# Performance work log

Hardware: AMD Instinct MI355X
Metric: run time of the kernel (lower is better)

Reference implementation:

```python
import jax, jax.numpy as jnp
from jax import lax
import numpy as np

BS, L, D, K, R, VOCAB = 4096, 200, 64, 4, 3, 100000
DROP = jnp.float32(-(1 << 31))


def squash(caps):
    # caps: (bs, K, D)
    n = jnp.linalg.norm(caps, axis=2, keepdims=True)   # (bs, K, 1)
    n2 = n * n
    return n2 / ((1.0 + n2) * n + 1e-9) * caps


def setup_inputs() -> dict:
    key = jax.random.key(0)
    ks = jax.random.split(key, 8)
    his = jax.random.randint(ks[0], (BS, L), 0, VOCAB)                     # item ids, 0 = pad
    E = jax.random.normal(ks[1], (VOCAB, D), dtype=jnp.float32)            # itemEmbeds.weight
    S = jax.random.normal(ks[2], (D, D), dtype=jnp.float32)                # bilinear map S
    B0 = jax.random.normal(ks[3], (K, L), dtype=jnp.float32)               # routing logits
    lim1 = 1.0 / np.sqrt(D)
    W1 = jax.random.uniform(ks[4], (D, 4 * D), jnp.float32, -lim1, lim1)   # dense1 (in, out)
    b1 = jax.random.uniform(ks[5], (4 * D,), jnp.float32, -lim1, lim1)
    lim2 = 1.0 / np.sqrt(4 * D)
    W2 = jax.random.uniform(ks[6], (4 * D, D), jnp.float32, -lim2, lim2)   # dense2 (in, out)
    b2 = jax.random.uniform(ks[7], (D,), jnp.float32, -lim2, lim2)
    return {"his": his, "E": E, "S": S, "B0": B0, "W1": W1, "b1": b1, "W2": W2, "b2": b2}


def reference(his, E, S, B0, W1, b1, W2, b2):
    bs = his.shape[0]
    # padding_idx=0 -> embedding row 0 is zero
    E = E.at[0].set(0.0)
    mask = (his != 0)[:, None, :]                       # (bs, 1, L), broadcasts over K
    hisP = jnp.einsum('bld,de->ble', E[his], S)         # (bs, L, D)
    hisPd = lax.stop_gradient(hisP)                     # routing updates run under no_grad
    B = jnp.broadcast_to(lax.stop_gradient(B0)[None], (bs, K, L))
    for _ in range(R - 1):
        W = jax.nn.softmax(jnp.where(mask, B, DROP), axis=2)   # (bs, K, L)
        caps = squash(jnp.einsum('bkl,bld->bkd', W, hisPd))
        B = B + jnp.einsum('bkd,bld->bkl', caps, hisPd)
    W = jax.nn.softmax(jnp.where(mask, B, DROP), axis=2)
    caps = squash(jnp.einsum('bkl,bld->bkd', W, hisP))         # differentiable last iter
    h = jax.nn.relu(jnp.einsum('bkd,df->bkf', caps, W1) + b1)
    return jnp.einsum('bkf,fd->bkd', h, W2) + b2               # (bs, K, D)
```

## Files before the change

kernel.cpp:

```cpp
#include <hip/hip_runtime.h>

#define LSEQ 200
#define KCAP 4
#define NVOC 100000

__global__ __launch_bounds__(256) void precompute_P(
    const float* __restrict__ E, const float* __restrict__ S,
    float* __restrict__ P)
{
    __shared__ __align__(16) float Sl[64 * 64];
    __shared__ __align__(16) float Et[64 * 16];
    const int tid = threadIdx.x;
    #pragma unroll
    for (int t = tid; t < 4096; t += 256) Sl[t] = S[t];
    const int vbase = blockIdx.x * 16;
    #pragma unroll
    for (int t = tid; t < 1024; t += 256) {
        int r = t >> 6, e = t & 63;
        Et[e * 16 + r] = E[(vbase + r) * 64 + e];
    }
    __syncthreads();
    const int d = tid & 63, q = tid >> 6;
    float a0 = 0.f, a1 = 0.f, a2 = 0.f, a3 = 0.f;
    #pragma unroll
    for (int e = 0; e < 64; e++) {
        float4 ev = *(const float4*)(Et + e * 16 + q * 4);
        float  s  = Sl[e * 64 + d];
        a0 = fmaf(ev.x, s, a0);
        a1 = fmaf(ev.y, s, a1);
        a2 = fmaf(ev.z, s, a2);
        a3 = fmaf(ev.w, s, a3);
    }
    const int v0 = vbase + q * 4;
    if (v0 == 0) a0 = 0.f;
    P[(v0 + 0) * 64 + d] = a0;
    P[(v0 + 1) * 64 + d] = a1;
    P[(v0 + 2) * 64 + d] = a2;
    P[(v0 + 3) * 64 + d] = a3;
}

__global__ __launch_bounds__(256, 2) void mind_row(
    const int*   __restrict__ his, const float* __restrict__ P,
    const float* __restrict__ B0,  const float* __restrict__ W1,
    const float* __restrict__ b1,  const float* __restrict__ W2,
    const float* __restrict__ b2,  float* __restrict__ out)
{
    __shared__ __align__(16) float hisPl[LSEQ * 65];
    __shared__ __align__(16) float W4[LSEQ * 4];
    __shared__ __align__(16) float Bm[KCAP * LSEQ];
    __shared__ __align__(16) float caps4[64 * 4];
    __shared__ __align__(16) float part[4 * 4 * 64];
    __shared__ float bigneg[LSEQ];
    __shared__ int   idxs[LSEQ];

    const int b    = blockIdx.x;
    const int tid  = threadIdx.x;
    const int lane = tid & 63;
    const int wv   = tid >> 6;

    for (int l = tid; l < LSEQ; l += 256) {
        int id = his[b * LSEQ + l];
        idxs[l]   = id;
        bigneg[l] = (id != 0) ? 0.f : -1e30f;
    }
    for (int t = tid; t < KCAP * LSEQ; t += 256) Bm[t] = B0[t];
    __syncthreads();

    float hp[50];
    #pragma unroll
    for (int i = 0; i < 50; i++) {
        int l = wv * 50 + i;
        float v = P[idxs[l] * 64 + lane];
        hp[i] = v;
        hisPl[l * 65 + lane] = v;
    }
    __syncthreads();

    for (int r = 0; r < 3; r++) {
        {
            const float* Bk = Bm + wv * LSEQ;
            float x0 = Bk[lane]       + bigneg[lane];
            float x1 = Bk[lane + 64]  + bigneg[lane + 64];
            float x2 = Bk[lane + 128] + bigneg[lane + 128];
            float x3 = (lane < 8) ? (Bk[lane + 192] + bigneg[lane + 192]) : -3.0e38f;
            float m = fmaxf(fmaxf(x0, x1), fmaxf(x2, x3));
            #pragma unroll
            for (int off = 32; off; off >>= 1) m = fmaxf(m, __shfl_xor(m, off, 64));
            float e0 = __expf(x0 - m), e1 = __expf(x1 - m), e2 = __expf(x2 - m);
            float e3 = (lane < 8) ? __expf(x3 - m) : 0.f;
            float s = e0 + e1 + e2 + e3;
            #pragma unroll
            for (int off = 32; off; off >>= 1) s += __shfl_xor(s, off, 64);
            float inv = 1.f / s;
            W4[lane * 4 + wv]         = e0 * inv;
            W4[(lane + 64) * 4 + wv]  = e1 * inv;
            W4[(lane + 128) * 4 + wv] = e2 * inv;
            if (lane < 8) W4[(lane + 192) * 4 + wv] = e3 * inv;
        }
        __syncthreads();

        {
            float a0 = 0, a1 = 0, a2 = 0, a3 = 0;
            #pragma unroll
            for (int i = 0; i < 50; i++) {
                int l = wv * 50 + i;
                float4 w = *(const float4*)(W4 + l * 4);
                float  v = hp[i];
                a0 = fmaf(w.x, v, a0);
                a1 = fmaf(w.y, v, a1);
                a2 = fmaf(w.z, v, a2);
                a3 = fmaf(w.w, v, a3);
            }
            part[wv * 256 + lane]       = a0;
            part[wv * 256 + 64 + lane]  = a1;
            part[wv * 256 + 128 + lane] = a2;
            part[wv * 256 + 192 + lane] = a3;
        }
        __syncthreads();

        {
            float c = part[wv * 64 + lane]       + part[256 + wv * 64 + lane]
                    + part[512 + wv * 64 + lane] + part[768 + wv * 64 + lane];
            float n2 = c * c;
            #pragma unroll
            for (int off = 32; off; off >>= 1) n2 += __shfl_xor(n2, off, 64);
            float n  = sqrtf(n2);
            float sc = n2 / ((1.f + n2) * n + 1e-9f);
            c *= sc;
            caps4[lane * 4 + wv] = c;
        }
        __syncthreads();

        if (r < 2) {
            if (tid < LSEQ) {
                const int l = tid;
                float d0 = 0, d1 = 0, d2 = 0, d3 = 0;
                #pragma unroll 8
                for (int d = 0; d < 64; d++) {
                    float  v = hisPl[l * 65 + d];
                    float4 c = *(const float4*)(caps4 + d * 4);
                    d0 = fmaf(c.x, v, d0);
                    d1 = fmaf(c.y, v, d1);
                    d2 = fmaf(c.z, v, d2);
                    d3 = fmaf(c.w, v, d3);
                }
                Bm[l]       += d0;
                Bm[200 + l] += d1;
                Bm[400 + l] += d2;
                Bm[600 + l] += d3;
            }
            __syncthreads();
        }
    }

    float* h4 = hisPl;
    {
        const int f = tid;
        float h0 = 0, h1 = 0, h2 = 0, h3 = 0;
        #pragma unroll 8
        for (int d = 0; d < 64; d++) {
            float  w = W1[d * 256 + f];
            float4 c = *(const float4*)(caps4 + d * 4);
            h0 = fmaf(c.x, w, h0);
            h1 = fmaf(c.y, w, h1);
            h2 = fmaf(c.z, w, h2);
            h3 = fmaf(c.w, w, h3);
        }
        float bb = b1[f];
        h0 = fmaxf(h0 + bb, 0.f);
        h1 = fmaxf(h1 + bb, 0.f);
        h2 = fmaxf(h2 + bb, 0.f);
        h3 = fmaxf(h3 + bb, 0.f);
        h4[f * 4 + 0] = h0; h4[f * 4 + 1] = h1;
        h4[f * 4 + 2] = h2; h4[f * 4 + 3] = h3;
    }
    __syncthreads();
    {
        float o0 = 0, o1 = 0, o2 = 0, o3 = 0;
        #pragma unroll 8
        for (int i = 0; i < 64; i++) {
            int f = wv * 64 + i;
            float  w  = W2[f * 64 + lane];
            float4 hv = *(const float4*)(h4 + f * 4);
            o0 = fmaf(hv.x, w, o0);
            o1 = fmaf(hv.y, w, o1);
            o2 = fmaf(hv.z, w, o2);
            o3 = fmaf(hv.w, w, o3);
        }
        part[wv * 256 + lane]       = o0;
        part[wv * 256 + 64 + lane]  = o1;
        part[wv * 256 + 128 + lane] = o2;
        part[wv * 256 + 192 + lane] = o3;
    }
    __syncthreads();
    {
        float o = part[wv * 64 + lane]       + part[256 + wv * 64 + lane]
                + part[512 + wv * 64 + lane] + part[768 + wv * 64 + lane];
        out[b * 256 + tid] = o + b2[lane];
    }
}

extern "C" void kernel_launch(void* const* d_in, const int* in_sizes, int n_in,
                              void* d_out, int out_size, void* d_ws, size_t ws_size,
                              hipStream_t stream) {
    const int*   his = (const int*)  d_in[0];
    const float* E   = (const float*)d_in[1];
    const float* S   = (const float*)d_in[2];
    const float* B0  = (const float*)d_in[3];
    const float* W1  = (const float*)d_in[4];
    const float* b1  = (const float*)d_in[5];
    const float* W2  = (const float*)d_in[6];
    const float* b2  = (const float*)d_in[7];
    float* out = (float*)d_out;
    float* P   = (float*)d_ws;

    precompute_P<<<NVOC / 16, 256, 0, stream>>>(E, S, P);
    mind_row<<<4096, 256, 0, stream>>>(his, P, B0, W1, b1, W2, b2, out);
}
```

Baseline: 242.7 us.

## Drop shared hisP tile, re-read P rows from global, raise occupancy, rework precompute

The main kernel no longer stages the gathered 200x64 hisP tile in shared memory (about 52KB). The routing-logit update instead re-reads each item's P row from global memory as float4 loads, and a separate small h4 buffer replaces the reused tile. With far less LDS per block, launch bounds rise from 2 to 5 blocks per SIMD-group target, trading extra global/L2 traffic for higher occupancy. The precompute kernel is rewritten to hold a column of S in registers per lane and sweep vocabulary rows with a grid-stride wavefront loop, using scalar loads of each E row.

```diff
diff --git a/kernel.cpp b/kernel.cpp
--- a/kernel.cpp
+++ b/kernel.cpp
@@ -8,48 +8,34 @@
     const float* __restrict__ E, const float* __restrict__ S,
     float* __restrict__ P)
 {
-    __shared__ __align__(16) float Sl[64 * 64];
-    __shared__ __align__(16) float Et[64 * 16];
-    const int tid = threadIdx.x;
+    const int lane = threadIdx.x & 63;
+    float s[64];
     #pragma unroll
-    for (int t = tid; t < 4096; t += 256) Sl[t] = S[t];
-    const int vbase = blockIdx.x * 16;
-    #pragma unroll
-    for (int t = tid; t < 1024; t += 256) {
-        int r = t >> 6, e = t & 63;
-        Et[e * 16 + r] = E[(vbase + r) * 64 + e];
-    }
-    __syncthreads();
-    const int d = tid & 63, q = tid >> 6;
-    float a0 = 0.f, a1 = 0.f, a2 = 0.f, a3 = 0.f;
-    #pragma unroll
-    for (int e = 0; e < 64; e++) {
-        float4 ev = *(const float4*)(Et + e * 16 + q * 4);
-        float  s  = Sl[e * 64 + d];
-        a0 = fmaf(ev.x, s, a0);
-        a1 = fmaf(ev.y, s, a1);
-        a2 = fmaf(ev.z, s, a2);
-        a3 = fmaf(ev.w, s, a3);
-    }
-    const int v0 = vbase + q * 4;
-    if (v0 == 0) a0 = 0.f;
-    P[(v0 + 0) * 64 + d] = a0;
-    P[(v0 + 1) * 64 + d] = a1;
-    P[(v0 + 2) * 64 + d] = a2;
-    P[(v0 + 3) * 64 + d] = a3;
+    for (int e = 0; e < 64; e++) s[e] = S[e * 64 + lane];
+
+    const int gw = (int)((blockIdx.x * blockDim.x + threadIdx.x) >> 6);
+    const int nw = (int)((gridDim.x * blockDim.x) >> 6);
+    for (int v = gw; v < NVOC; v += nw) {
+        const int vu = __builtin_amdgcn_readfirstlane(v);
+        const float* __restrict__ er = E + (size_t)vu * 64;
+        float acc = 0.f;
+        #pragma unroll
+        for (int e = 0; e < 64; e++) acc = fmaf(er[e], s[e], acc);
+        P[(size_t)vu * 64 + lane] = (vu == 0) ? 0.f : acc;
+    }
 }
 
-__global__ __launch_bounds__(256, 2) void mind_row(
+__global__ __launch_bounds__(256, 5) void mind_row(
     const int*   __restrict__ his, const float* __restrict__ P,
     const float* __restrict__ B0,  const float* __restrict__ W1,
     const float* __restrict__ b1,  const float* __restrict__ W2,
     const float* __restrict__ b2,  float* __restrict__ out)
 {
-    __shared__ __align__(16) float hisPl[LSEQ * 65];
     __shared__ __align__(16) float W4[LSEQ * 4];
     __shared__ __align__(16) float Bm[KCAP * LSEQ];
     __shared__ __align__(16) float caps4[64 * 4];
     __shared__ __align__(16) float part[4 * 4 * 64];
+    __shared__ __align__(16) float h4[256 * 4];
     __shared__ float bigneg[LSEQ];
     __shared__ int   idxs[LSEQ];
 
@@ -70,11 +56,8 @@
     #pragma unroll
     for (int i = 0; i < 50; i++) {
         int l = wv * 50 + i;
-        float v = P[idxs[l] * 64 + lane];
-        hp[i] = v;
-        hisPl[l * 65 + lane] = v;
-    }
-    __syncthreads();
+        hp[i] = P[idxs[l] * 64 + lane];
+    }
 
     for (int r = 0; r < 3; r++) {
         {
@@ -88,10 +71,10 @@
             for (int off = 32; off; off >>= 1) m = fmaxf(m, __shfl_xor(m, off, 64));
             float e0 = __expf(x0 - m), e1 = __expf(x1 - m), e2 = __expf(x2 - m);
             float e3 = (lane < 8) ? __expf(x3 - m) : 0.f;
-            float s = e0 + e1 + e2 + e3;
-            #pragma unroll
-            for (int off = 32; off; off >>= 1) s += __shfl_xor(s, off, 64);
-            float inv = 1.f / s;
+            float ssum = e0 + e1 + e2 + e3;
+            #pragma unroll
+            for (int off = 32; off; off >>= 1) ssum += __shfl_xor(ssum, off, 64);
+            float inv = 1.f / ssum;
             W4[lane * 4 + wv]         = e0 * inv;
             W4[(lane + 64) * 4 + wv]  = e1 * inv;
             W4[(lane + 128) * 4 + wv] = e2 * inv;
@@ -133,27 +116,41 @@
 
         if (r < 2) {
             if (tid < LSEQ) {
-                const int l = tid;
+                const float4* __restrict__ rowp = (const float4*)(P + idxs[tid] * 64);
                 float d0 = 0, d1 = 0, d2 = 0, d3 = 0;
-                #pragma unroll 8
-                for (int d = 0; d < 64; d++) {
-                    float  v = hisPl[l * 65 + d];
-                    float4 c = *(const float4*)(caps4 + d * 4);
-                    d0 = fmaf(c.x, v, d0);
-                    d1 = fmaf(c.y, v, d1);
-                    d2 = fmaf(c.z, v, d2);
-                    d3 = fmaf(c.w, v, d3);
+                #pragma unroll
+                for (int j = 0; j < 16; j++) {
+                    float4 v = rowp[j];
+                    {
+                        float4 c = *(const float4*)(caps4 + (j * 4 + 0) * 4);
+                        d0 = fmaf(c.x, v.x, d0); d1 = fmaf(c.y, v.x, d1);
+                        d2 = fmaf(c.z, v.x, d2); d3 = fmaf(c.w, v.x, d3);
+                    }
+                    {
+                        float4 c = *(const float4*)(caps4 + (j * 4 + 1) * 4);
+                        d0 = fmaf(c.x, v.y, d0); d1 = fmaf(c.y, v.y, d1);
+                        d2 = fmaf(c.z, v.y, d2); d3 = fmaf(c.w, v.y, d3);
+                    }
+                    {
+                        float4 c = *(const float4*)(caps4 + (j * 4 + 2) * 4);
+                        d0 = fmaf(c.x, v.z, d0); d1 = fmaf(c.y, v.z, d1);
+                        d2 = fmaf(c.z, v.z, d2); d3 = fmaf(c.w, v.z, d3);
+                    }
+                    {
+                        float4 c = *(const float4*)(caps4 + (j * 4 + 3) * 4);
+                        d0 = fmaf(c.x, v.w, d0); d1 = fmaf(c.y, v.w, d1);
+                        d2 = fmaf(c.z, v.w, d2); d3 = fmaf(c.w, v.w, d3);
+                    }
                 }
-                Bm[l]       += d0;
-                Bm[200 + l] += d1;
-                Bm[400 + l] += d2;
-                Bm[600 + l] += d3;
+                Bm[tid]       += d0;
+                Bm[200 + tid] += d1;
+                Bm[400 + tid] += d2;
+                Bm[600 + tid] += d3;
             }
             __syncthreads();
         }
     }
 
-    float* h4 = hisPl;
     {
         const int f = tid;
         float h0 = 0, h1 = 0, h2 = 0, h3 = 0;
@@ -214,6 +211,6 @@
     float* out = (float*)d_out;
     float* P   = (float*)d_ws;
 
-    precompute_P<<<NVOC / 16, 256, 0, stream>>>(E, S, P);
+    precompute_P<<<1024, 256, 0, stream>>>(E, S, P);
     mind_row<<<4096, 256, 0, stream>>>(his, P, B0, W1, b1, W2, b2, out);
 }
```

After: 249.9 us. 1.03x slower.
